# Kernel tuning notes

Hardware: AMD Instinct MI355X
Metric: run time of the kernel (lower is better)

## Reference

```python
import jax, jax.numpy as jnp
import numpy as np


def _gcn_conv(x, src, dst, W, b, n):
    """PyG GCNConv with default settings: add self-loops, symmetric norm, bias after agg.
    out = D^{-1/2} (A + I) D^{-1/2} (x @ W) + b
    """
    h = x @ W  # [N, out]
    # degree of A+I with unit edge weights: 1 (self-loop) + in-degree on dst
    deg = jnp.ones((n,), x.dtype).at[dst].add(jnp.ones((dst.shape[0],), x.dtype))
    dinv = jax.lax.rsqrt(deg)  # [N]
    coef = dinv[src] * dinv[dst]  # [E]
    agg = jax.ops.segment_sum(h[src] * coef[:, None], dst, num_segments=n)
    # self-loop contribution: norm = dinv[i]*dinv[i]
    return agg + h * (dinv * dinv)[:, None] + b


def setup_inputs() -> dict:
    key = jax.random.key(0)
    ks = jax.random.split(key, 10)
    N, E, D, H1, H2 = 100000, 2500000, 128, 32, 64
    x = jax.random.normal(ks[0], (N, D), jnp.float32)
    ei = jax.random.randint(ks[1], (2, E), 0, N, dtype=jnp.int32)
    # GCN layer params (glorot-ish scale)
    W1c = jax.random.normal(ks[2], (D, H1), jnp.float32) / np.sqrt(D)
    b1c = jnp.zeros((H1,), jnp.float32)
    W2c = jax.random.normal(ks[3], (H1, H2), jnp.float32) / np.sqrt(H1)
    b2c = jnp.zeros((H2,), jnp.float32)
    # MLP head: Linear(H2,H2) -> ReLU -> Linear(H2,1)
    Wm1 = jax.random.normal(ks[4], (H2, H2), jnp.float32) / np.sqrt(H2)
    bm1 = jnp.zeros((H2,), jnp.float32)
    Wm2 = jax.random.normal(ks[5], (H2, 1), jnp.float32) / np.sqrt(H2)
    bm2 = jnp.zeros((1,), jnp.float32)
    return {"x": x, "W1c": W1c, "b1c": b1c, "W2c": W2c, "b2c": b2c,
            "Wm1": Wm1, "bm1": bm1, "Wm2": Wm2, "bm2": bm2,
            "ei": ei, "num_nodes": 50000}


def reference(x, W1c, b1c, W2c, b2c, Wm1, bm1, Wm2, bm2, ei, num_nodes):
    src, dst = ei[0], ei[1]
    n = x.shape[0]
    z = jax.nn.relu(_gcn_conv(x, src, dst, W1c, b1c, n))
    z = jax.nn.relu(_gcn_conv(z, src, dst, W2c, b2c, n))
    v = jax.nn.relu(z @ Wm1 + bm1) @ Wm2 + bm2  # [N, 1]
    nbatches = n // num_nodes
    # mean per-graph state value (reshape over stacked graphs, mean over nodes)
    return v.reshape(nbatches, num_nodes).mean(axis=1)
```

## Files before the change

kernel.cpp:

```cpp
#include <hip/hip_runtime.h>


typedef _Float16 half_t;
typedef __attribute__((ext_vector_type(8))) _Float16 half8;
typedef __attribute__((ext_vector_type(4))) float f32x4;
typedef __attribute__((ext_vector_type(2))) float f32x2;
typedef __attribute__((ext_vector_type(4))) int   i32x4;

#define CHUNK 4096
#define BKN   512
#define NBMAX 256

__global__ void k_zero_out(float* out, int n) {
    int i = blockIdx.x * blockDim.x + threadIdx.x;
    if (i < n) out[i] = 0.0f;
}

__device__ __forceinline__ int sfull(const int* S, const int* bs, int j) {
    return (j == 0) ? 0 : S[j] + bs[(j - 1) >> 8];
}


__global__ __launch_bounds__(256) void k_count_coarse(
    const int* __restrict__ dst, int* __restrict__ table, int E, int nblk, int NB)
{
    __shared__ int cnt[NBMAX];
    const int tid = threadIdx.x;
    for (int i = tid; i < NB; i += 256) cnt[i] = 0;
    __syncthreads();
    const int base = blockIdx.x * CHUNK;
    const int lim = min(CHUNK, E - base);
    if (lim == CHUNK) {
        const int4* d4 = (const int4*)(dst + base);
        for (int i = tid; i < CHUNK / 4; i += 256) {
            int4 v = d4[i];
            atomicAdd(&cnt[v.x >> 9], 1);
            atomicAdd(&cnt[v.y >> 9], 1);
            atomicAdd(&cnt[v.z >> 9], 1);
            atomicAdd(&cnt[v.w >> 9], 1);
        }
    } else {
        for (int i = tid; i < lim; i += 256) atomicAdd(&cnt[dst[base + i] >> 9], 1);
    }
    __syncthreads();
    for (int b = tid; b < NB; b += 256) table[b * nblk + blockIdx.x] = cnt[b];
}

__global__ __launch_bounds__(256) void k_scan1(const int* __restrict__ cnts, int* __restrict__ S,
                                               int* __restrict__ bsums, int T) {
    __shared__ int sh[256];
    int t = threadIdx.x;
    int i = blockIdx.x * 256 + t;
    int v = (i < T) ? cnts[i] : 0;
    sh[t] = v;
    __syncthreads();
    for (int off = 1; off < 256; off <<= 1) {
        int tv = (t >= off) ? sh[t - off] : 0;
        __syncthreads();
        sh[t] += tv;
        __syncthreads();
    }
    if (i < T) S[i + 1] = sh[t];
    if (t == 255) bsums[blockIdx.x] = sh[255];
}

__global__ __launch_bounds__(1024) void k_scan2(int* bs, int nb) {
    __shared__ int sh[1024];
    int t = threadIdx.x;
    int v = (t < nb) ? bs[t] : 0;
    sh[t] = v;
    __syncthreads();
    for (int off = 1; off < 1024; off <<= 1) {
        int tv = (t >= off) ? sh[t - off] : 0;
        __syncthreads();
        sh[t] += tv;
        __syncthreads();
    }
    if (t < nb) bs[t] = sh[t] - v;
}

__global__ __launch_bounds__(256) void k_scatter2(
    const int* __restrict__ ei, const int* __restrict__ S, const int* __restrict__ bsums,
    int* __restrict__ codes, int E, int nblk, int NB)
{
    __shared__ int cur[NBMAX];
    const int tid = threadIdx.x;
    for (int i = tid; i < NB; i += 256)
        cur[i] = sfull(S, bsums, i * nblk + blockIdx.x);
    __syncthreads();
    const int base = blockIdx.x * CHUNK;
    const int lim = min(CHUNK, E - base);
    if (lim == CHUNK) {
        const int4* s4 = (const int4*)(ei + base);
        const int4* d4 = (const int4*)(ei + E + base);
        for (int i = tid; i < CHUNK / 4; i += 256) {
            int4 sv = s4[i], dv = d4[i];
            { int pos = atomicAdd(&cur[dv.x >> 9], 1); codes[pos] = ((dv.x & 511) << 17) | sv.x; }
            { int pos = atomicAdd(&cur[dv.y >> 9], 1); codes[pos] = ((dv.y & 511) << 17) | sv.y; }
            { int pos = atomicAdd(&cur[dv.z >> 9], 1); codes[pos] = ((dv.z & 511) << 17) | sv.z; }
            { int pos = atomicAdd(&cur[dv.w >> 9], 1); codes[pos] = ((dv.w & 511) << 17) | sv.w; }
        }
    } else {
        for (int i = tid; i < lim; i += 256) {
            int e = base + i;
            int s = ei[e], d = ei[E + e];
            int pos = atomicAdd(&cur[d >> 9], 1);
            codes[pos] = ((d & 511) << 17) | s;
        }
    }
}

__global__ __launch_bounds__(512) void k_fine(
    const int* __restrict__ codes, const int* __restrict__ S, const int* __restrict__ bsums,
    int* __restrict__ esrc, int* __restrict__ row_start,
    float* __restrict__ dinv, int nblk, int N, int E, int NB)
{
    __shared__ int cnt[BKN];
    __shared__ int sh[BKN];
    __shared__ int cur[BKN];
    const int tid = threadIdx.x;
    cnt[tid] = 0;
    __syncthreads();
    const int b = blockIdx.x;
    const int beg = sfull(S, bsums, b * nblk), end = sfull(S, bsums, (b + 1) * nblk);
    for (int e = beg + tid; e < end; e += 512) atomicAdd(&cnt[codes[e] >> 17], 1);
    __syncthreads();
    sh[tid] = cnt[tid];
    __syncthreads();
    for (int off = 1; off < 512; off <<= 1) {
        int tv = (tid >= off) ? sh[tid - off] : 0;
        __syncthreads();
        sh[tid] += tv;
        __syncthreads();
    }
    {
        int fs = beg + sh[tid] - cnt[tid];
        cur[tid] = fs;
        int n = b * BKN + tid;
        if (n < N) {
            row_start[n] = fs;
            dinv[n] = rsqrtf(1.0f + (float)cnt[tid]);
        }
    }
    if (b == NB - 1 && tid == 0) row_start[N] = E;
    __syncthreads();
    for (int e = beg + tid; e < end; e += 512) {
        int c = codes[e];
        int pos = atomicAdd(&cur[c >> 17], 1);
        esrc[pos] = c & 0x1FFFF;
    }
}


__global__ __launch_bounds__(256) void k_prep(
    const float* __restrict__ W1, const float* __restrict__ W2, const float* __restrict__ Wm1,
    half_t* __restrict__ W1t, half_t* __restrict__ W2t, half_t* __restrict__ Wm1t,
    float* __restrict__ out, int out_n)
{
    int i = blockIdx.x * 256 + threadIdx.x;
    if (i < 128 * 32) { int k = i >> 5, c = i & 31; W1t[c * 128 + k] = (half_t)W1[i]; }
    if (i < 32 * 64)  { int k = i >> 6, c = i & 63; W2t[c * 32 + k]  = (half_t)W2[i]; }
    if (i < 64 * 64)  { int k = i >> 6, c = i & 63; Wm1t[c * 64 + k] = (half_t)Wm1[i]; }
    if (i < out_n) out[i] = 0.0f;
}

__global__ __launch_bounds__(256) void k_gemm1_mfma(
    const float* __restrict__ x, const half_t* __restrict__ W1t,
    const float* __restrict__ dinv, unsigned char* __restrict__ hs8, int N)
{
    const int tid = threadIdx.x;
    const int wid = tid >> 6, lane = tid & 63;
    const int quad = lane >> 4, n16 = lane & 15;
    const int n0 = blockIdx.x * 64 + wid * 16;
    if (n0 >= N) return;
    const int nrow = min(n0 + n16, N - 1);
    const float* xr = x + (size_t)nrow * 128;
    f32x4 acc0 = {0.f, 0.f, 0.f, 0.f}, acc1 = {0.f, 0.f, 0.f, 0.f};
#pragma unroll
    for (int kc = 0; kc < 4; ++kc) {
        float4 f0 = *(const float4*)(xr + kc * 32 + quad * 8);
        float4 f1 = *(const float4*)(xr + kc * 32 + quad * 8 + 4);
        half8 a;
        a[0] = (half_t)f0.x; a[1] = (half_t)f0.y; a[2] = (half_t)f0.z; a[3] = (half_t)f0.w;
        a[4] = (half_t)f1.x; a[5] = (half_t)f1.y; a[6] = (half_t)f1.z; a[7] = (half_t)f1.w;
        half8 b0 = *(const half8*)(W1t + (size_t)n16 * 128 + kc * 32 + quad * 8);
        half8 b1 = *(const half8*)(W1t + (size_t)(16 + n16) * 128 + kc * 32 + quad * 8);
        acc0 = __builtin_amdgcn_mfma_f32_16x16x32_f16(a, b0, acc0, 0, 0, 0);
        acc1 = __builtin_amdgcn_mfma_f32_16x16x32_f16(a, b1, acc1, 0, 0, 0);
    }
#pragma unroll
    for (int r = 0; r < 4; ++r) {
        int n = n0 + quad * 4 + r;
        if (n < N) {
            float dv = dinv[n];
            int w0 = __builtin_amdgcn_cvt_pk_fp8_f32(acc0[r] * dv, 0.f, 0, false);
            int w1 = __builtin_amdgcn_cvt_pk_fp8_f32(acc1[r] * dv, 0.f, 0, false);
            hs8[(size_t)n * 32 + n16]      = (unsigned char)(w0 & 0xFF);
            hs8[(size_t)n * 32 + 16 + n16] = (unsigned char)(w1 & 0xFF);
        }
    }
}

__device__ __forceinline__ void unpack_dw(int w, float* acc) {
    f32x2 p;
    p = __builtin_amdgcn_cvt_pk_f32_fp8(w, false); acc[0] += p.x; acc[1] += p.y;
    p = __builtin_amdgcn_cvt_pk_f32_fp8(w, true);  acc[2] += p.x; acc[3] += p.y;
}

__device__ __forceinline__ void unpack_acc16(i32x4 w, float* acc) {
    unpack_dw(w.x, acc + 0);
    unpack_dw(w.y, acc + 4);
    unpack_dw(w.z, acc + 8);
    unpack_dw(w.w, acc + 12);
}

__device__ __forceinline__ void gather_row16(
    const int* __restrict__ row_start, const int* __restrict__ esrc,
    const int* __restrict__ IN, int n, int l, float* acc)
{
    const int beg = row_start[n], end = row_start[n + 1];
    {
        i32x4 ws_ = *(const i32x4*)(IN + (size_t)n * 8 + l * 4);
        unpack_acc16(ws_, acc);
    }
    int e = beg;
    for (; e + 3 < end; e += 4) {
        int s0 = __builtin_nontemporal_load(esrc + e);
        int s1 = __builtin_nontemporal_load(esrc + e + 1);
        int s2 = __builtin_nontemporal_load(esrc + e + 2);
        int s3 = __builtin_nontemporal_load(esrc + e + 3);
        i32x4 w0 = *(const i32x4*)(IN + (size_t)s0 * 8 + l * 4);
        i32x4 w1 = *(const i32x4*)(IN + (size_t)s1 * 8 + l * 4);
        i32x4 w2 = *(const i32x4*)(IN + (size_t)s2 * 8 + l * 4);
        i32x4 w3 = *(const i32x4*)(IN + (size_t)s3 * 8 + l * 4);
        unpack_acc16(w0, acc);
        unpack_acc16(w1, acc);
        unpack_acc16(w2, acc);
        unpack_acc16(w3, acc);
    }
    for (; e < end; ++e) {
        int s = __builtin_nontemporal_load(esrc + e);
        i32x4 w = *(const i32x4*)(IN + (size_t)s * 8 + l * 4);
        unpack_acc16(w, acc);
    }
}

__global__ __launch_bounds__(128) void k_agg8_l1(
    const int* __restrict__ row_start, const int* __restrict__ esrc,
    const int* __restrict__ IN, const float* __restrict__ bias,
    const float* __restrict__ dinv, int* __restrict__ OUT, int N)
{
    const int tid = threadIdx.x;
    const int g = tid >> 1, l = tid & 1;
    const int n = blockIdx.x * 64 + g;
    if (n >= N) return;
    float acc[16];
#pragma unroll
    for (int j = 0; j < 16; ++j) acc[j] = 0.f;
    gather_row16(row_start, esrc, IN, n, l, acc);
    const float dv = dinv[n];
    float v[16];
#pragma unroll
    for (int j = 0; j < 16; ++j)
        v[j] = fmaxf(dv * acc[j] + bias[l * 16 + j], 0.f) * dv;
    i32x4 o;
    {
        int d;
        d = __builtin_amdgcn_cvt_pk_fp8_f32(v[0],  v[1],  0, false);
        d = __builtin_amdgcn_cvt_pk_fp8_f32(v[2],  v[3],  d, true);  o.x = d;
        d = __builtin_amdgcn_cvt_pk_fp8_f32(v[4],  v[5],  0, false);
        d = __builtin_amdgcn_cvt_pk_fp8_f32(v[6],  v[7],  d, true);  o.y = d;
        d = __builtin_amdgcn_cvt_pk_fp8_f32(v[8],  v[9],  0, false);
        d = __builtin_amdgcn_cvt_pk_fp8_f32(v[10], v[11], d, true);  o.z = d;
        d = __builtin_amdgcn_cvt_pk_fp8_f32(v[12], v[13], 0, false);
        d = __builtin_amdgcn_cvt_pk_fp8_f32(v[14], v[15], d, true);  o.w = d;
    }
    __builtin_nontemporal_store(o, (i32x4*)(OUT + (size_t)n * 8 + l * 4));
}

__global__ __launch_bounds__(128) void k_agg8_tail(
    const int* __restrict__ row_start, const int* __restrict__ esrc,
    const int* __restrict__ IN, const float* __restrict__ dinv,
    const half_t* __restrict__ W2t, const float* __restrict__ b2,
    const half_t* __restrict__ Wm1t, const float* __restrict__ bm1,
    const float* __restrict__ Wm2, const float* __restrict__ bm2,
    const int* __restrict__ nn_p, float* __restrict__ out, int N, int n_graphs)
{
    __shared__ float gacc[32];
    __shared__ __align__(16) half_t Yb[64][40];
    __shared__ __align__(16) half_t Hb[2][16][72];
    const int tid = threadIdx.x;
    if (tid < 32) gacc[tid] = 0.f;
    {
        const int g = tid >> 1, l = tid & 1;
        const int n = blockIdx.x * 64 + g;
        if (n < N) {
            float acc[16];
#pragma unroll
            for (int j = 0; j < 16; ++j) acc[j] = 0.f;
            gather_row16(row_start, esrc, IN, n, l, acc);
            const float dv = dinv[n];
#pragma unroll
            for (int j = 0; j < 16; ++j) Yb[g][l * 16 + j] = (half_t)(dv * acc[j]);
        } else {
#pragma unroll
            for (int j = 0; j < 16; ++j) Yb[g][l * 16 + j] = (half_t)0.f;
        }
    }
    __syncthreads();
    const int wid = tid >> 6, lane = tid & 63;
    const int quad = lane >> 4, n16 = lane & 15;
    const int nnv = nn_p[0];
    const float bm2v = bm2[0];
#pragma unroll
    for (int t2 = 0; t2 < 2; ++t2) {
        const int n0 = blockIdx.x * 64 + wid * 32 + t2 * 16;
        if (n0 >= N) break;
        half8 a1 = *(const half8*)&Yb[wid * 32 + t2 * 16 + n16][quad * 8];
        f32x4 acc1[4];
#pragma unroll
        for (int t = 0; t < 4; ++t) {
            half8 bf = *(const half8*)(W2t + (size_t)(t * 16 + n16) * 32 + quad * 8);
            f32x4 z = {0.f, 0.f, 0.f, 0.f};
            acc1[t] = __builtin_amdgcn_mfma_f32_16x16x32_f16(a1, bf, z, 0, 0, 0);
        }
#pragma unroll
        for (int t = 0; t < 4; ++t) {
            int c = t * 16 + n16;
            float bb = b2[c];
#pragma unroll
            for (int r = 0; r < 4; ++r)
                Hb[wid][quad * 4 + r][c] = (half_t)fmaxf(acc1[t][r] + bb, 0.f);
        }
        half8 a2lo = *(const half8*)&Hb[wid][n16][quad * 8];
        half8 a2hi = *(const half8*)&Hb[wid][n16][32 + quad * 8];
        f32x4 acc2[4];
#pragma unroll
        for (int t = 0; t < 4; ++t) {
            half8 b0 = *(const half8*)(Wm1t + (size_t)(t * 16 + n16) * 64 + quad * 8);
            half8 b1 = *(const half8*)(Wm1t + (size_t)(t * 16 + n16) * 64 + 32 + quad * 8);
            f32x4 a = {0.f, 0.f, 0.f, 0.f};
            a = __builtin_amdgcn_mfma_f32_16x16x32_f16(a2lo, b0, a, 0, 0, 0);
            a = __builtin_amdgcn_mfma_f32_16x16x32_f16(a2hi, b1, a, 0, 0, 0);
            acc2[t] = a;
        }
        float vsum[4] = {0.f, 0.f, 0.f, 0.f};
#pragma unroll
        for (int t = 0; t < 4; ++t) {
            int c = t * 16 + n16;
            float bb = bm1[c], ww = Wm2[c];
#pragma unroll
            for (int r = 0; r < 4; ++r)
                vsum[r] += fmaxf(acc2[t][r] + bb, 0.f) * ww;
        }
#pragma unroll
        for (int m = 1; m < 16; m <<= 1) {
#pragma unroll
            for (int r = 0; r < 4; ++r) vsum[r] += __shfl_xor(vsum[r], m, 64);
        }
        if (n16 == 0) {
#pragma unroll
            for (int r = 0; r < 4; ++r) {
                int n = n0 + quad * 4 + r;
                if (n < N) {
                    int g = n / nnv;
                    if (g < 32) atomicAdd(&gacc[g], vsum[r] + bm2v);
                }
            }
        }
    }
    __syncthreads();
    if (tid < n_graphs && tid < 32) atomicAdd(&out[tid], gacc[tid] / (float)nnv);
}

__global__ void k_zero_int(int* p, int n) {
    int i = blockIdx.x * blockDim.x + threadIdx.x;
    if (i < n) p[i] = 0;
}
__global__ void k_hist(const int* __restrict__ dst, int* __restrict__ deg, int E) {
    int e = blockIdx.x * blockDim.x + threadIdx.x;
    if (e < E) atomicAdd(&deg[dst[e]], 1);
}
__global__ void k_dinv(const int* __restrict__ deg, float* __restrict__ dinv, int n) {
    int i = blockIdx.x * blockDim.x + threadIdx.x;
    if (i < n) dinv[i] = rsqrtf(1.0f + (float)deg[i]);
}
__global__ __launch_bounds__(256) void k_gemm1f(
    const float* __restrict__ x, const float* __restrict__ W,
    const float* __restrict__ dinv, float* __restrict__ hs1, int N)
{
    __shared__ float Wl[128 * 32];
    __shared__ __align__(16) float Xl[8 * 132];
    const int tid = threadIdx.x;
    for (int i = tid; i < 128 * 32; i += 256) Wl[i] = W[i];
    const int node0 = blockIdx.x * 8;
    {
        int r = tid >> 5, c4 = tid & 31;
        int node = node0 + r;
        float4 v = make_float4(0.f, 0.f, 0.f, 0.f);
        if (node < N) v = ((const float4*)(x + (size_t)node * 128))[c4];
        *(float4*)&Xl[r * 132 + c4 * 4] = v;
    }
    __syncthreads();
    const int row = tid >> 5, f = tid & 31;
    float acc = 0.f;
#pragma unroll
    for (int k = 0; k < 128; k += 4) {
        float4 xv = *(const float4*)&Xl[row * 132 + k];
        acc += xv.x * Wl[(k + 0) * 32 + f];
        acc += xv.y * Wl[(k + 1) * 32 + f];
        acc += xv.z * Wl[(k + 2) * 32 + f];
        acc += xv.w * Wl[(k + 3) * 32 + f];
    }
    const int node = node0 + row;
    if (node < N) hs1[(size_t)node * 32 + f] = acc * dinv[node];
}
__global__ __launch_bounds__(256) void k_gemm2(
    const float* __restrict__ agg1, const float* __restrict__ W,
    const float* __restrict__ dinv, float* __restrict__ hs2, int N)
{
    __shared__ float Wl[32 * 64];
    __shared__ __align__(16) float Zl[4 * 36];
    const int tid = threadIdx.x;
    for (int i = tid; i < 32 * 64; i += 256) Wl[i] = W[i];
    const int node0 = blockIdx.x * 4;
    if (tid < 128) {
        int r = tid >> 5, c = tid & 31;
        int node = node0 + r;
        float v = 0.f;
        if (node < N) v = fmaxf(agg1[(size_t)node * 32 + c], 0.f);
        Zl[r * 36 + c] = v;
    }
    __syncthreads();
    const int row = tid >> 6, f = tid & 63;
    float acc = 0.f;
#pragma unroll
    for (int k = 0; k < 32; k += 4) {
        float4 zv = *(const float4*)&Zl[row * 36 + k];
        acc += zv.x * Wl[(k + 0) * 64 + f];
        acc += zv.y * Wl[(k + 1) * 64 + f];
        acc += zv.z * Wl[(k + 2) * 64 + f];
        acc += zv.w * Wl[(k + 3) * 64 + f];
    }
    int node = node0 + row;
    if (node < N) hs2[(size_t)node * 64 + f] = acc * dinv[node];
}
template <int F>
__global__ void k_agg_init(const float* __restrict__ hs, const float* __restrict__ b,
                           const float* __restrict__ dinv, float* __restrict__ agg, int N)
{
    long long t = (long long)blockIdx.x * blockDim.x + threadIdx.x;
    int n = (int)(t / F), f = (int)(t % F);
    if (n < N) agg[(size_t)n * F + f] = hs[(size_t)n * F + f] * dinv[n] + b[f];
}
template <int F>
__global__ void k_edge_atomic(const int* __restrict__ ei, const float* __restrict__ hs,
                              const float* __restrict__ dinv, float* __restrict__ agg, int E)
{
    long long tid = (long long)blockIdx.x * blockDim.x + threadIdx.x;
    int e = (int)(tid / F), f = (int)(tid % F);
    if (e < E) {
        int s = ei[e], d = ei[E + e];
        atomicAdd(&agg[(size_t)d * F + f], hs[(size_t)s * F + f] * dinv[d]);
    }
}
__global__ __launch_bounds__(256) void k_mlp(
    const float* __restrict__ agg2, const float* __restrict__ Wm1,
    const float* __restrict__ bm1, const float* __restrict__ Wm2,
    const float* __restrict__ bm2, float* __restrict__ vout, int N)
{
    __shared__ float Wl[64 * 64];
    __shared__ float W2l[64];
    __shared__ __align__(16) float Zl[4][64];
    const int tid = threadIdx.x;
    for (int i = tid; i < 64 * 64; i += 256) Wl[i] = Wm1[i];
    if (tid < 64) W2l[tid] = Wm2[tid];
    const int wid = tid >> 6, lane = tid & 63;
    const int node = blockIdx.x * 4 + wid;
    float zv = 0.f;
    if (node < N) zv = fmaxf(agg2[(size_t)node * 64 + lane], 0.f);
    Zl[wid][lane] = zv;
    __syncthreads();
    float t = bm1[lane];
#pragma unroll
    for (int k = 0; k < 64; k += 4) {
        float4 z4 = *(const float4*)&Zl[wid][k];
        t += z4.x * Wl[(k + 0) * 64 + lane];
        t += z4.y * Wl[(k + 1) * 64 + lane];
        t += z4.z * Wl[(k + 2) * 64 + lane];
        t += z4.w * Wl[(k + 3) * 64 + lane];
    }
    t = fmaxf(t, 0.f);
    float val = t * W2l[lane];
#pragma unroll
    for (int off = 32; off > 0; off >>= 1) val += __shfl_down(val, off, 64);
    if (lane == 0 && node < N) vout[node] = val + bm2[0];
}
__global__ void k_reduce(const float* __restrict__ v, const int* __restrict__ num_nodes_p,
                         float* out, int N, int n_graphs)
{
    __shared__ float acc[32];
    int tid = threadIdx.x;
    if (tid < n_graphs) acc[tid] = 0.f;
    __syncthreads();
    int i = blockIdx.x * blockDim.x + tid;
    int nn = num_nodes_p[0];
    if (i < N) {
        int g = i / nn;
        if (g < n_graphs) atomicAdd(&acc[g], v[i]);
    }
    __syncthreads();
    if (tid < n_graphs) atomicAdd(&out[tid], acc[tid] / (float)nn);
}

extern "C" void kernel_launch(void* const* d_in, const int* in_sizes, int n_in,
                              void* d_out, int out_size, void* d_ws, size_t ws_size,
                              hipStream_t stream)
{
    const float* x   = (const float*)d_in[0];
    const float* W1  = (const float*)d_in[1];
    const float* b1  = (const float*)d_in[2];
    const float* W2  = (const float*)d_in[3];
    const float* b2  = (const float*)d_in[4];
    const float* Wm1 = (const float*)d_in[5];
    const float* bm1 = (const float*)d_in[6];
    const float* Wm2 = (const float*)d_in[7];
    const float* bm2 = (const float*)d_in[8];
    const int*   ei  = (const int*)d_in[9];
    const int*   nn  = (const int*)d_in[10];
    const int N = in_sizes[0] / 128;
    const int E = in_sizes[9] / 2;
    float* out = (float*)d_out;

    const int NB = (N + BKN - 1) / BKN;
    const int nblk = (E + CHUNK - 1) / CHUNK;
    const long long T = (long long)NB * nblk;
    const int nb1 = (int)((T + 255) / 256);
    auto al4 = [](size_t v) { return (v + 3) & ~(size_t)3; };
    const size_t need_ints = al4(T) + al4(T + 1) + 1024 + al4(E) + al4(E)
                           + al4(N + 1) + al4(N) + 8ull * N + 8ull * N
                           + 5120 + 64;
    const bool use_new = (N <= 131072) && (T <= 262144) && (nb1 <= 1024)
                       && (NB <= NBMAX) && (out_size <= 32)
                       && (ws_size >= need_ints * sizeof(int));

    if (use_new) {
        int* w = (int*)d_ws;
        int*    table     = w;                          w += al4(T);
        int*    S         = w;                          w += al4(T + 1);
        int*    bsums     = w;                          w += 1024;
        int*    codes     = w;                          w += al4(E);
        int*    esrc      = w;                          w += al4(E);
        int*    row_start = w;                          w += al4(N + 1);
        float*  dinv      = (float*)w;                  w += al4(N);
        int*    hs8       = w;                          w += 8ull * N;
        int*    Zs8       = w;                          w += 8ull * N;
        half_t* W1t       = (half_t*)w;
        half_t* W2t       = W1t + 4096;
        half_t* Wm1t      = W2t + 2048;

        k_count_coarse<<<nblk, 256, 0, stream>>>(ei + E, table, E, nblk, NB);
        k_scan1<<<nb1, 256, 0, stream>>>(table, S, bsums, (int)T);
        k_scan2<<<1, 1024, 0, stream>>>(bsums, nb1);
        k_scatter2<<<nblk, 256, 0, stream>>>(ei, S, bsums, codes, E, nblk, NB);
        k_fine<<<NB, 512, 0, stream>>>(codes, S, bsums, esrc, row_start, dinv, nblk, N, E, NB);
        k_prep<<<16, 256, 0, stream>>>(W1, W2, Wm1, W1t, W2t, Wm1t, out, out_size);
        k_gemm1_mfma<<<(N + 63) / 64, 256, 0, stream>>>(x, W1t, dinv, (unsigned char*)hs8, N);
        k_agg8_l1<<<(N + 63) / 64, 128, 0, stream>>>(row_start, esrc, hs8, b1, dinv, Zs8, N);
        k_agg8_tail<<<(N + 63) / 64, 128, 0, stream>>>(row_start, esrc, Zs8, dinv,
                                                       W2t, b2, Wm1t, bm1, Wm2, bm2,
                                                       nn, out, N, out_size);
    } else {
        const size_t Ns = (size_t)N;
        float* dinv = (float*)d_ws;
        float* B    = dinv + N;
        float* hs1  = B;
        float* agg1 = B + 32 * Ns;
        float* hs2  = B + 64 * Ns;
        float* agg2 = B + 128 * Ns;
        float* vtmp = B;
        int*   deg  = (int*)B;

        const int nb = (N + 255) / 256;
        k_zero_out<<<1, 64, 0, stream>>>(out, out_size);
        k_zero_int<<<nb, 256, 0, stream>>>(deg, N);
        k_hist<<<(E + 255) / 256, 256, 0, stream>>>(ei + E, deg, E);
        k_dinv<<<nb, 256, 0, stream>>>(deg, dinv, N);
        k_gemm1f<<<(N + 7) / 8, 256, 0, stream>>>(x, W1, dinv, hs1, N);
        {
            long long t = (long long)N * 32;
            k_agg_init<32><<<(unsigned)((t + 255) / 256), 256, 0, stream>>>(hs1, b1, dinv, agg1, N);
            t = (long long)E * 32;
            k_edge_atomic<32><<<(unsigned)((t + 255) / 256), 256, 0, stream>>>(ei, hs1, dinv, agg1, E);
        }
        k_gemm2<<<(N + 3) / 4, 256, 0, stream>>>(agg1, W2, dinv, hs2, N);
        {
            long long t = (long long)N * 64;
            k_agg_init<64><<<(unsigned)((t + 255) / 256), 256, 0, stream>>>(hs2, b2, dinv, agg2, N);
            t = (long long)E * 64;
            k_edge_atomic<64><<<(unsigned)((t + 255) / 256), 256, 0, stream>>>(ei, hs2, dinv, agg2, E);
        }
        k_mlp<<<(N + 3) / 4, 256, 0, stream>>>(agg2, Wm1, bm1, Wm2, bm2, vtmp, N);
        k_reduce<<<nb, 256, 0, stream>>>(vtmp, nn, out, N, out_size);
    }
}
```

Before: 244.9 us.

## Split each node's edge gather across two thread pairs and reduce via shuffle

The two aggregation kernels now assign four threads per node instead of two, and each half handles half the node's edge range. The partial sums are combined with a lane xor shuffle. Block size doubles to 256, and the tail kernel's MFMA stage is remapped to four waves of 16 nodes each. The goal is more memory-level parallelism and shorter per-thread dependency chains in the latency-bound fp8 gather, at the cost of extra shuffles and half the threads sitting idle in the epilogue.

```diff
diff --git a/kernel.cpp b/kernel.cpp
--- a/kernel.cpp
+++ b/kernel.cpp
@@ -214,17 +214,12 @@
     unpack_dw(w.w, acc + 12);
 }
 
-__device__ __forceinline__ void gather_row16(
-    const int* __restrict__ row_start, const int* __restrict__ esrc,
-    const int* __restrict__ IN, int n, int l, float* acc)
-{
-    const int beg = row_start[n], end = row_start[n + 1];
-    {
-        i32x4 ws_ = *(const i32x4*)(IN + (size_t)n * 8 + l * 4);
-        unpack_acc16(ws_, acc);
-    }
-    int e = beg;
-    for (; e + 3 < end; e += 4) {
+__device__ __forceinline__ void gather_range16(
+    const int* __restrict__ esrc, const int* __restrict__ IN,
+    int from, int to, int l, float* acc)
+{
+    int e = from;
+    for (; e + 3 < to; e += 4) {
         int s0 = __builtin_nontemporal_load(esrc + e);
         int s1 = __builtin_nontemporal_load(esrc + e + 1);
         int s2 = __builtin_nontemporal_load(esrc + e + 2);
@@ -238,26 +233,44 @@
         unpack_acc16(w2, acc);
         unpack_acc16(w3, acc);
     }
-    for (; e < end; ++e) {
+    for (; e < to; ++e) {
         int s = __builtin_nontemporal_load(esrc + e);
         i32x4 w = *(const i32x4*)(IN + (size_t)s * 8 + l * 4);
         unpack_acc16(w, acc);
     }
 }
 
-__global__ __launch_bounds__(128) void k_agg8_l1(
+__device__ __forceinline__ void gather_node16(
+    const int* __restrict__ row_start, const int* __restrict__ esrc,
+    const int* __restrict__ IN, int n, int l, int h, float* acc)
+{
+    const int beg = row_start[n], end = row_start[n + 1];
+    const int mid = (beg + end) >> 1;
+    if (h == 0) {
+        i32x4 ws_ = *(const i32x4*)(IN + (size_t)n * 8 + l * 4);
+        unpack_acc16(ws_, acc);
+        gather_range16(esrc, IN, beg, mid, l, acc);
+    } else {
+        gather_range16(esrc, IN, mid, end, l, acc);
+    }
+#pragma unroll
+    for (int j = 0; j < 16; ++j) acc[j] += __shfl_xor(acc[j], 2, 64);
+}
+
+__global__ __launch_bounds__(256) void k_agg8_l1(
     const int* __restrict__ row_start, const int* __restrict__ esrc,
     const int* __restrict__ IN, const float* __restrict__ bias,
     const float* __restrict__ dinv, int* __restrict__ OUT, int N)
 {
     const int tid = threadIdx.x;
-    const int g = tid >> 1, l = tid & 1;
+    const int g = tid >> 2, l = tid & 1, h = (tid >> 1) & 1;
     const int n = blockIdx.x * 64 + g;
     if (n >= N) return;
     float acc[16];
 #pragma unroll
     for (int j = 0; j < 16; ++j) acc[j] = 0.f;
-    gather_row16(row_start, esrc, IN, n, l, acc);
+    gather_node16(row_start, esrc, IN, n, l, h, acc);
+    if (h != 0) return;
     const float dv = dinv[n];
     float v[16];
 #pragma unroll
@@ -278,7 +291,7 @@
     __builtin_nontemporal_store(o, (i32x4*)(OUT + (size_t)n * 8 + l * 4));
 }
 
-__global__ __launch_bounds__(128) void k_agg8_tail(
+__global__ __launch_bounds__(256) void k_agg8_tail(
     const int* __restrict__ row_start, const int* __restrict__ esrc,
     const int* __restrict__ IN, const float* __restrict__ dinv,
     const half_t* __restrict__ W2t, const float* __restrict__ b2,
@@ -288,21 +301,23 @@
 {
     __shared__ float gacc[32];
     __shared__ __align__(16) half_t Yb[64][40];
-    __shared__ __align__(16) half_t Hb[2][16][72];
+    __shared__ __align__(16) half_t Hb[4][16][72];
     const int tid = threadIdx.x;
     if (tid < 32) gacc[tid] = 0.f;
     {
-        const int g = tid >> 1, l = tid & 1;
+        const int g = tid >> 2, l = tid & 1, h = (tid >> 1) & 1;
         const int n = blockIdx.x * 64 + g;
         if (n < N) {
             float acc[16];
 #pragma unroll
             for (int j = 0; j < 16; ++j) acc[j] = 0.f;
-            gather_row16(row_start, esrc, IN, n, l, acc);
-            const float dv = dinv[n];
-#pragma unroll
-            for (int j = 0; j < 16; ++j) Yb[g][l * 16 + j] = (half_t)(dv * acc[j]);
-        } else {
+            gather_node16(row_start, esrc, IN, n, l, h, acc);
+            if (h == 0) {
+                const float dv = dinv[n];
+#pragma unroll
+                for (int j = 0; j < 16; ++j) Yb[g][l * 16 + j] = (half_t)(dv * acc[j]);
+            }
+        } else if (h == 0) {
 #pragma unroll
             for (int j = 0; j < 16; ++j) Yb[g][l * 16 + j] = (half_t)0.f;
         }
@@ -312,11 +327,9 @@
     const int quad = lane >> 4, n16 = lane & 15;
     const int nnv = nn_p[0];
     const float bm2v = bm2[0];
-#pragma unroll
-    for (int t2 = 0; t2 < 2; ++t2) {
-        const int n0 = blockIdx.x * 64 + wid * 32 + t2 * 16;
-        if (n0 >= N) break;
-        half8 a1 = *(const half8*)&Yb[wid * 32 + t2 * 16 + n16][quad * 8];
+    const int n0 = blockIdx.x * 64 + wid * 16;
+    if (n0 < N) {
+        half8 a1 = *(const half8*)&Yb[wid * 16 + n16][quad * 8];
         f32x4 acc1[4];
 #pragma unroll
         for (int t = 0; t < 4; ++t) {
@@ -566,8 +579,8 @@
         k_fine<<<NB, 512, 0, stream>>>(codes, S, bsums, esrc, row_start, dinv, nblk, N, E, NB);
         k_prep<<<16, 256, 0, stream>>>(W1, W2, Wm1, W1t, W2t, Wm1t, out, out_size);
         k_gemm1_mfma<<<(N + 63) / 64, 256, 0, stream>>>(x, W1t, dinv, (unsigned char*)hs8, N);
-        k_agg8_l1<<<(N + 63) / 64, 128, 0, stream>>>(row_start, esrc, hs8, b1, dinv, Zs8, N);
-        k_agg8_tail<<<(N + 63) / 64, 128, 0, stream>>>(row_start, esrc, Zs8, dinv,
+        k_agg8_l1<<<(N + 63) / 64, 256, 0, stream>>>(row_start, esrc, hs8, b1, dinv, Zs8, N);
+        k_agg8_tail<<<(N + 63) / 64, 256, 0, stream>>>(row_start, esrc, Zs8, dinv,
                                                        W2t, b2, Wm1t, bm1, Wm2, bm2,
                                                        nn, out, N, out_size);
     } else {
```

Measured after the change: 256.1 us. +4.6%, slower.
